# Performance work log

Hardware: AMD Instinct MI355X
Metric: run time of the kernel (lower is better)

The kernel has to match this reference:

```python
import jax, jax.numpy as jnp
import numpy as np


def setup_inputs() -> dict:
    key = jax.random.key(0)
    ks = jax.random.split(key, 10)
    B, C1, C2, Co, H, W = 4, 128, 128, 128, 64, 64
    Cin = C1 + C2
    delta_p_processed = jax.random.normal(ks[0], (B, C1, H, W), jnp.float32)
    delta_f_hist = jax.random.normal(ks[1], (B, C2, H, W), jnp.float32)
    Wq = jax.random.normal(ks[2], (Co, Cin), jnp.float32) * 0.02
    bq = jax.random.normal(ks[3], (Co,), jnp.float32) * 0.02
    Wk = jax.random.normal(ks[4], (Co, Cin), jnp.float32) * 0.02
    bk = jax.random.normal(ks[5], (Co,), jnp.float32) * 0.02
    Wv = jax.random.normal(ks[6], (Co, Cin), jnp.float32) * 0.02
    bv = jax.random.normal(ks[7], (Co,), jnp.float32) * 0.02
    Wg = jax.random.normal(ks[8], (Co, Co), jnp.float32) * 0.02
    bg = jnp.zeros((Co,), jnp.float32)
    gamma = jnp.array([0.5], jnp.float32)
    return {
        "delta_p_processed": delta_p_processed,
        "delta_f_hist": delta_f_hist,
        "Wq": Wq, "bq": bq, "Wk": Wk, "bk": bk,
        "Wv": Wv, "bv": bv, "Wg": Wg, "bg": bg,
        "gamma": gamma,
    }


def reference(delta_p_processed, delta_f_hist, Wq, bq, Wk, bk, Wv, bv, Wg, bg, gamma):
    x = jnp.concatenate([delta_p_processed, delta_f_hist], axis=1)  # (B, Cin, H, W)
    B, Cin, H, W = x.shape
    Co = Wq.shape[0]
    N = H * W
    xf = x.reshape(B, Cin, N)
    # 1x1 convs == per-pixel linear projections
    q = jnp.einsum('oc,bcn->bno', Wq, xf) + bq          # (B, N, Co)
    k = jnp.einsum('oc,bcn->bon', Wk, xf) + bk[:, None]  # (B, Co, N)
    v = jnp.einsum('oc,bcn->bno', Wv, xf) + bv          # (B, N, Co)
    scale = 1.0 / (Co ** 0.5)
    attn = jax.nn.softmax(jnp.einsum('bno,bom->bnm', q, k) * scale, axis=-1)  # (B, N, N)
    out_attn = jnp.einsum('bnm,bmo->bno', attn, v)      # (B, N, Co)
    out_attn = out_attn.transpose(0, 2, 1).reshape(B, Co, H, W)
    gate = jax.nn.sigmoid(
        jnp.einsum('oc,bchw->bohw', Wg, out_attn) + bg[None, :, None, None]
    )
    residual = x[:, :Co, :, :]
    return gamma[0] * gate * out_attn + (1.0 - gate) * residual
```

## Files before the change

### kernel.cpp

```cpp
#include <hip/hip_runtime.h>
#include <stdint.h>

#define B_    4
#define CIN   256
#define CO    128
#define NPOS  4096

typedef float  f4      __attribute__((ext_vector_type(4)));
typedef float  f2      __attribute__((ext_vector_type(2)));
typedef float  f32x16  __attribute__((ext_vector_type(16)));
typedef int    int4v   __attribute__((ext_vector_type(4)));
typedef short  short4v __attribute__((ext_vector_type(4)));
typedef short  short8v __attribute__((ext_vector_type(8)));
typedef __bf16 bf16x8  __attribute__((ext_vector_type(8)));

#if __has_builtin(__builtin_amdgcn_exp2f)
#define EXP2(x) __builtin_amdgcn_exp2f(x)
#else
#define EXP2(x) exp2f(x)
#endif

static __device__ __forceinline__ unsigned short f2bf(float f){
  union { float f; unsigned int u; } v; v.f = f;
  unsigned int u = v.u + 0x7FFFu + ((v.u >> 16) & 1u);
  return (unsigned short)(u >> 16);
}
static __device__ __forceinline__ float bf2f(unsigned short h){
  union { unsigned int u; float f; } v; v.u = ((unsigned int)h) << 16;
  return v.f;
}
static __device__ __forceinline__ unsigned int cvt_pk_bf16(float lo, float hi){
  unsigned int r;
  asm("v_cvt_pk_bf16_f32 %0, %1, %2" : "=v"(r) : "v"(lo), "v"(hi));
  return r;
}

static __device__ __forceinline__ void half_swap_pair(float v, float& x, float& y){
  union { float f; int i; } a; a.f = v;
  auto r = __builtin_amdgcn_permlane32_swap(a.i, a.i, false, false);
  union { int i; float f; } o0, o1; o0.i = (int)r[0]; o1.i = (int)r[1];
  x = o0.f; y = o1.f;
}

__global__ __launch_bounds__(64) void wconv_kernel(
    const float* __restrict__ Wq, const float* __restrict__ Wk,
    const float* __restrict__ Wv, const float* __restrict__ Wg,
    unsigned short* __restrict__ Wf)
{
  int blk = blockIdx.x, l = threadIdx.x;
  const float* W; int o, c; int stride;
  if (blk < 192){
    int ob = blk >> 4, cs = blk & 15;
    int mat = ob >> 2, obl = ob & 3;
    W = (mat == 0) ? Wq : ((mat == 1) ? Wk : Wv);
    o = obl * 32 + (l & 31); c = cs * 16 + (l >> 5) * 8; stride = 256;
  } else {
    int idx = blk - 192;
    int ob = idx >> 3, cs = idx & 7;
    W = Wg;
    o = ob * 32 + (l & 31); c = cs * 16 + (l >> 5) * 8; stride = 128;
  }
  const float* src = W + (size_t)o * stride + c;
  f4 a = *(const f4*)src, bb = *(const f4*)(src + 4);
  short8v pk;
  #pragma unroll
  for (int j = 0; j < 4; ++j){ pk[j] = (short)f2bf(a[j]); pk[4+j] = (short)f2bf(bb[j]); }
  *(short8v*)(Wf + ((size_t)blk * 64 + l) * 8) = pk;
}

__global__ __launch_bounds__(256) void qkv_kernel(
    const float* __restrict__ dp, const float* __restrict__ df,
    const unsigned short* __restrict__ Wf,
    const float* __restrict__ bq, const float* __restrict__ bk,
    const float* __restrict__ bv,
    unsigned short* __restrict__ Qf, unsigned short* __restrict__ Kf,
    unsigned short* __restrict__ Vf)
{
  __shared__ unsigned int xs4[32 * 128];

  int t  = threadIdx.x;
  int b  = blockIdx.x >> 7;
  int kt = blockIdx.x & 127;
  int n0 = kt * 32;

  {
    int cp = t & 127, nh = t >> 7;
    int c0 = cp * 2, c1 = c0 + 1;
    const float* s0 = (c0 < 128) ? dp + ((size_t)b*128 + c0) * NPOS
                                 : df + ((size_t)b*128 + (c0-128)) * NPOS;
    const float* s1 = (c1 < 128) ? dp + ((size_t)b*128 + c1) * NPOS
                                 : df + ((size_t)b*128 + (c1-128)) * NPOS;
    f4 x0[4], x1[4];
    #pragma unroll
    for (int i = 0; i < 4; ++i){
      x0[i] = *(const f4*)(s0 + n0 + nh*16 + i*4);
      x1[i] = *(const f4*)(s1 + n0 + nh*16 + i*4);
    }
    #pragma unroll
    for (int i = 0; i < 16; ++i){
      int n = nh * 16 + i;
      unsigned int pk = cvt_pk_bf16(x0[i>>2][i&3], x1[i>>2][i&3]);
      int chunk = (cp >> 2) ^ (n & 7);
      xs4[n * 128 + chunk * 4 + (cp & 3)] = pk;
    }
  }
  __syncthreads();

  int w = t >> 6, l = t & 63;
  int lo5 = l & 31, h = l >> 5;

  f32x16 acc[3] = {};
  const unsigned short* WfL = Wf + (size_t)l * 8;

  #pragma unroll 4
  for (int cs = 0; cs < 16; ++cs){
    bf16x8 xf = *(const bf16x8*)((const char*)xs4 +
                 (size_t)(lo5 * 512 + (((cs*2 + h) ^ (lo5 & 7)) * 16)));
    #pragma unroll
    for (int i = 0; i < 3; ++i){
      int ob = w * 3 + i;
      bf16x8 wf = *(const bf16x8*)(WfL + ((size_t)ob * 16 + cs) * 512);
      if (ob < 8) acc[i] = __builtin_amdgcn_mfma_f32_32x32x16_bf16(wf, xf, acc[i], 0, 0, 0);
      else        acc[i] = __builtin_amdgcn_mfma_f32_32x32x16_bf16(xf, wf, acc[i], 0, 0, 0);
    }
  }

  const float kScale = 0.12751743f;
  #pragma unroll
  for (int i = 0; i < 3; ++i){
    int ob = w * 3 + i, mat = ob >> 2, obl = ob & 3;
    if (mat < 2){
      const float* bias = (mat == 0) ? bq : bk;
      unsigned short* dst = ((mat == 0) ? Qf : Kf) + (size_t)(b*128 + kt) * 4096;
      #pragma unroll
      for (int r1 = 0; r1 < 4; ++r1){
        f4 b4 = *(const f4*)(bias + obl*32 + r1*8 + h*4);
        float v0 = acc[i][r1*4+0] + b4[0], v1 = acc[i][r1*4+1] + b4[1];
        float v2 = acc[i][r1*4+2] + b4[2], v3 = acc[i][r1*4+3] + b4[3];
        if (mat == 0){ v0 *= kScale; v1 *= kScale; v2 *= kScale; v3 *= kScale; }
        union { unsigned int u[2]; short4v s; } pk;
        pk.u[0] = cvt_pk_bf16(v0, v1); pk.u[1] = cvt_pk_bf16(v2, v3);
        int ci = obl * 2 + (r1 >> 1);
        size_t si = (size_t)ci * 512 + (size_t)(lo5 + 32*(r1 & 1)) * 8 + 4*h;
        *(short4v*)(dst + si) = pk.s;
      }
    } else {
      float bvl = bv[obl * 32 + lo5];
      unsigned short* dst = Vf + ((size_t)(b*128 + kt) * 8 + obl*2) * 512;
      #pragma unroll
      for (int r1 = 0; r1 < 4; ++r1){
        union { unsigned int u[2]; short4v s; } pk;
        pk.u[0] = cvt_pk_bf16(acc[i][r1*4+0] + bvl, acc[i][r1*4+1] + bvl);
        pk.u[1] = cvt_pk_bf16(acc[i][r1*4+2] + bvl, acc[i][r1*4+3] + bvl);
        size_t si = (size_t)(r1 >> 1) * 512 + (size_t)(lo5 + 32*(r1 & 1)) * 8 + 4*h;
        *(short4v*)(dst + si) = pk.s;
      }
    }
  }
}

#define ATTN_TILE(K0, CUR, NXT)                                                 \
  {                                                                             \
    f32x16 sA = {}, sB = {};                                                    \
    __builtin_amdgcn_s_setprio(1);                                              \
    _Pragma("unroll")                                                           \
    for (int ci = 0; ci < 4; ++ci){                                             \
      sA = __builtin_amdgcn_mfma_f32_32x32x16_bf16(kf[CUR][2*ci],   qf[2*ci],   sA, 0, 0, 0); \
      sB = __builtin_amdgcn_mfma_f32_32x32x16_bf16(kf[CUR][2*ci+1], qf[2*ci+1], sB, 0, 0, 0); \
    }                                                                           \
    __builtin_amdgcn_s_setprio(0);                                              \
                    \
    {                                                                           \
      int kn_ = (K0) + 32; if (kn_ >= kend) kn_ = kbeg;                         \
      size_t tb_ = (size_t)(kn_ >> 5) * 4096;                                   \
      _Pragma("unroll")                                                         \
      for (int ci = 0; ci < 8; ++ci)                                            \
        kf[NXT][ci] = *(const bf16x8*)(KfL + tb_ + ci * 512);                   \
      _Pragma("unroll")                                                         \
      for (int fi = 0; fi < 8; ++fi)                                            \
        vf[NXT][fi] = *(const bf16x8*)(VfL + tb_ + fi * 512);                   \
    }                                                                           \
    f32x16 sv = sA + sB;                                                        \
    float a0_ = fmaxf(fmaxf(sv[0],  sv[1]),  sv[2]);                            \
    float a1_ = fmaxf(fmaxf(sv[3],  sv[4]),  sv[5]);                            \
    float a2_ = fmaxf(fmaxf(sv[6],  sv[7]),  sv[8]);                            \
    float a3_ = fmaxf(fmaxf(sv[9],  sv[10]), sv[11]);                           \
    float a4_ = fmaxf(fmaxf(sv[12], sv[13]), sv[14]);                           \
    float vm  = fmaxf(fmaxf(fmaxf(fmaxf(a0_, a1_), a2_), fmaxf(a3_, a4_)), sv[15]); \
    { float xx_, yy_; half_swap_pair(vm, xx_, yy_);                             \
      vm = fmaxf(vm, fmaxf(xx_, yy_)); }                                        \
    if (!__all(vm <= m_run + 8.0f)){                                            \
      float m_new = fmaxf(m_run, vm);                                           \
      float alpha = EXP2(m_run - m_new);                                        \
      _Pragma("unroll")                                                         \
      for (int ob = 0; ob < 4; ++ob){                                           \
        _Pragma("unroll")                                                       \
        for (int i = 0; i < 16; ++i) oacc[ob][i] *= alpha;                      \
      }                                                                         \
      l_run *= alpha;                                                           \
      m_run = m_new;                                                            \
    }                                                                           \
    float p[16];                                                                \
    _Pragma("unroll")                                                           \
    for (int i = 0; i < 16; ++i) p[i] = EXP2(sv[i] - m_run);                    \
    float t0 = (p[0]  + p[1])  + (p[2]  + p[3]);                                \
    float t1 = (p[4]  + p[5])  + (p[6]  + p[7]);                                \
    float t2 = (p[8]  + p[9])  + (p[10] + p[11]);                               \
    float t3 = (p[12] + p[13]) + (p[14] + p[15]);                               \
    float ts = (t0 + t1) + (t2 + t3);                                           \
    { float xx_, yy_; half_swap_pair(ts, xx_, yy_); ts = xx_ + yy_; }           \
    l_run += ts;                                                                \
    unsigned int pw[8];                                                         \
    _Pragma("unroll")                                                           \
    for (int i = 0; i < 8; ++i) pw[i] = cvt_pk_bf16(p[2*i], p[2*i+1]);          \
    auto r20 = __builtin_amdgcn_permlane32_swap((int)pw[2], (int)pw[0], false, false); \
    auto r31 = __builtin_amdgcn_permlane32_swap((int)pw[3], (int)pw[1], false, false); \
    auto r64v = __builtin_amdgcn_permlane32_swap((int)pw[6], (int)pw[4], false, false); \
    auto r75 = __builtin_amdgcn_permlane32_swap((int)pw[7], (int)pw[5], false, false); \
    union { int4v i4; bf16x8 b; } pb0, pb1;                                     \
    pb0.i4 = (int4v){(int)r20[1],  (int)r31[1], (int)r20[0],  (int)r31[0]};     \
    pb1.i4 = (int4v){(int)r64v[1], (int)r75[1], (int)r64v[0], (int)r75[0]};     \
    __builtin_amdgcn_s_setprio(1);                                              \
    _Pragma("unroll")                                                           \
    for (int ob = 0; ob < 4; ++ob){                                             \
      oacc[ob] = __builtin_amdgcn_mfma_f32_32x32x16_bf16(vf[CUR][2*ob],   pb0.b, oacc[ob], 0, 0, 0); \
      oacc[ob] = __builtin_amdgcn_mfma_f32_32x32x16_bf16(vf[CUR][2*ob+1], pb1.b, oacc[ob], 0, 0, 0); \
    }                                                                           \
    __builtin_amdgcn_s_setprio(0);                                              \
  }

__global__ __launch_bounds__(256) void attn_kernel(
    const unsigned short* __restrict__ Qf, const unsigned short* __restrict__ Kf,
    const unsigned short* __restrict__ Vf, float* __restrict__ OP,
    f2* __restrict__ ML, int SPLIT, int CHUNK)
{
  int t    = threadIdx.x;
  int b    = blockIdx.x >> 7;
  int qb   = blockIdx.x & 127;
  int w    = t >> 6;
  int l    = t & 63;
  int lq   = l & 31;
  int h    = l >> 5;
  int q0   = qb * 32;
  int s    = w;

  const unsigned short* QfL = Qf + (size_t)b * (128 * 8 * 512) + (size_t)l * 8;
  size_t qtb = (size_t)qb * 4096;
  bf16x8 qf[8];
  #pragma unroll
  for (int ci = 0; ci < 8; ++ci) qf[ci] = *(const bf16x8*)(QfL + qtb + ci * 512);

  const unsigned short* KfL = Kf + (size_t)b * (128 * 8 * 512) + (size_t)l * 8;
  const unsigned short* VfL = Vf + (size_t)b * (128 * 8 * 512) + (size_t)l * 8;

  f32x16 oacc[4] = {};
  float m_run = -3.0e38f, l_run = 0.f;

  const int kbeg = s * CHUNK;
  const int kend = kbeg + CHUNK;

  bf16x8 kf[2][8];
  bf16x8 vf[2][8];
  {
    size_t tb0 = (size_t)(kbeg >> 5) * 4096;
    #pragma unroll
    for (int ci = 0; ci < 8; ++ci) kf[0][ci] = *(const bf16x8*)(KfL + tb0 + ci * 512);
    #pragma unroll
    for (int fi = 0; fi < 8; ++fi) vf[0][fi] = *(const bf16x8*)(VfL + tb0 + fi * 512);
  }

  const int NIT = CHUNK >> 5;
  for (int it = 0; it < NIT; it += 2){
    int k0a = kbeg + it * 32;
    ATTN_TILE(k0a, 0, 1)
    int k0b = k0a + 32;
    ATTN_TILE(k0b, 1, 0)
  }

  float* Ob = OP + (((size_t)b * NPOS + q0 + lq) * SPLIT + s) * 128 + h * 4;
  #pragma unroll
  for (int ob = 0; ob < 4; ++ob){
    #pragma unroll
    for (int rg = 0; rg < 4; ++rg){
      f4 vv;
      vv[0] = oacc[ob][rg*4+0]; vv[1] = oacc[ob][rg*4+1];
      vv[2] = oacc[ob][rg*4+2]; vv[3] = oacc[ob][rg*4+3];
      *(f4*)(Ob + ob * 32 + rg * 8) = vv;
    }
  }
  if (h == 0){
    f2 ml; ml[0] = m_run; ml[1] = l_run;
    ML[((size_t)b * NPOS + q0 + lq) * SPLIT + s] = ml;
  }
}

__global__ __launch_bounds__(256) void gate_kernel(
    const float* __restrict__ OP, const f2* __restrict__ ML,
    const unsigned short* __restrict__ Wf,
    const float* __restrict__ bg,
    const float* __restrict__ gamma, const float* __restrict__ dp,
    float* __restrict__ out, int SPLIT)
{
  __shared__ float        oat[128 * 33];
  __shared__ unsigned int xs[32 * 64];
  __shared__ float        wsm[32 * 8];

  int t  = threadIdx.x;
  int b  = blockIdx.x >> 7;
  int nt = blockIdx.x & 127;
  int n0 = nt * 32;

  if (t < 32){
    size_t mlb = ((size_t)b * NPOS + n0 + t) * SPLIT;
    float mmax = -3.0e38f;
    for (int sp = 0; sp < SPLIT; ++sp) mmax = fmaxf(mmax, ML[mlb + sp][0]);
    float L = 0.f;
    for (int sp = 0; sp < SPLIT; ++sp) L += ML[mlb + sp][1] * EXP2(ML[mlb + sp][0] - mmax);
    float Linv = 1.0f / L;
    for (int sp = 0; sp < SPLIT; ++sp)
      wsm[t * 8 + sp] = EXP2(ML[mlb + sp][0] - mmax) * Linv;
  }
  __syncthreads();

  int w = t >> 6, l = t & 63;

  #pragma unroll
  for (int i = 0; i < 8; ++i){
    int n = w * 8 + i;
    const f2* op = (const f2*)(OP + (((size_t)b * NPOS + n0 + n) * SPLIT) * 128) + l;
    float a0 = 0.f, a1 = 0.f;
    for (int sp = 0; sp < SPLIT; ++sp){
      f2 v = op[sp * 64];
      float ww = wsm[n * 8 + sp];
      a0 += ww * v[0]; a1 += ww * v[1];
    }
    oat[(2*l)   * 33 + n] = a0;
    oat[(2*l+1) * 33 + n] = a1;
    xs[n * 64 + (((l >> 2) ^ (n & 7)) << 2) + (l & 3)] = cvt_pk_bf16(a0, a1);
  }
  __syncthreads();

  int lq = l & 31, h = l >> 5;
  f32x16 acc = {};
  const unsigned short* WgfL = Wf + (size_t)(192 + w * 8) * 512 + (size_t)l * 8;
  #pragma unroll
  for (int cs = 0; cs < 8; ++cs){
    bf16x8 xf = *(const bf16x8*)((const char*)xs +
                 (size_t)(lq * 256 + (((cs*2 + h) ^ (lq & 7)) * 16)));
    bf16x8 wgf = *(const bf16x8*)(WgfL + (size_t)cs * 512);
    acc = __builtin_amdgcn_mfma_f32_32x32x16_bf16(wgf, xf, acc, 0, 0, 0);
  }

  float gm = gamma[0];
  const float kLog2e = 1.4426950408889634f;
  #pragma unroll
  for (int r1 = 0; r1 < 4; ++r1){
    f4 b4 = *(const f4*)(bg + w*32 + r1*8 + h*4);
    #pragma unroll
    for (int j = 0; j < 4; ++j){
      int o = w*32 + r1*8 + h*4 + j;
      float garg = acc[r1*4 + j] + b4[j];
      float gate = 1.0f / (1.0f + EXP2(-kLog2e * garg));
      float oa = oat[o * 33 + lq];
      size_t gi = ((size_t)b * 128 + o) * NPOS + n0 + lq;
      float rs = dp[gi];
      out[gi] = gm * gate * oa + (1.0f - gate) * rs;
    }
  }
}

extern "C" void kernel_launch(void* const* d_in, const int* in_sizes, int n_in,
                              void* d_out, int out_size, void* d_ws, size_t ws_size,
                              hipStream_t stream)
{
  (void)in_sizes; (void)n_in; (void)out_size;
  const float* dp    = (const float*)d_in[0];
  const float* df    = (const float*)d_in[1];
  const float* Wq    = (const float*)d_in[2];
  const float* bq    = (const float*)d_in[3];
  const float* Wk    = (const float*)d_in[4];
  const float* bk    = (const float*)d_in[5];
  const float* Wv    = (const float*)d_in[6];
  const float* bv    = (const float*)d_in[7];
  const float* Wg    = (const float*)d_in[8];
  const float* bg    = (const float*)d_in[9];
  const float* gamma = (const float*)d_in[10];

  const int SPLIT = 4;
  const int CHUNK = NPOS / SPLIT;

  unsigned short* Qf = (unsigned short*)d_ws;
  unsigned short* Kf = Qf + (size_t)B_ * NPOS * 128;
  unsigned short* Vf = Kf + (size_t)B_ * NPOS * 128;
  float*          OP = (float*)(Vf + (size_t)B_ * NPOS * 128);
  f2*             ML = (f2*)(OP + (size_t)B_ * NPOS * SPLIT * 128);
  unsigned short* Wf = (unsigned short*)(ML + (size_t)B_ * NPOS * SPLIT);
  float*          out = (float*)d_out;
  (void)ws_size;

  wconv_kernel<<<dim3(224), dim3(64), 0, stream>>>(Wq, Wk, Wv, Wg, Wf);
  qkv_kernel<<<dim3(B_ * 128), dim3(256), 0, stream>>>(dp, df, Wf, bq, bk, bv, Qf, Kf, Vf);
  attn_kernel<<<dim3(B_ * 128), dim3(256), 0, stream>>>(Qf, Kf, Vf, OP, ML, SPLIT, CHUNK);
  gate_kernel<<<dim3(B_ * 128), dim3(256), 0, stream>>>(OP, ML, Wf, bg, gamma, dp, out, SPLIT);
}
```

Before: 96.31 us.

## Process two query tiles per wave to reuse K/V fragments

The attention kernel now has each wave compute two 32-row query tiles against the same loaded K and V fragments, keeping separate softmax running stats and accumulators for each tile. This halves the K/V global loads per unit of MFMA work and interleaves independent MFMA chains. The grid is halved, so fewer waves run per CU, and register pressure roughly doubles, which could cause spills or lower occupancy.

```diff
diff --git a/kernel.cpp b/kernel.cpp
--- a/kernel.cpp
+++ b/kernel.cpp
@@ -159,14 +159,16 @@
   }
 }
 
-#define ATTN_TILE(K0, CUR, NXT)                                                 \
+#define ATTN_TILE2(K0, CUR, NXT)                                                \
   {                                                                             \
-    f32x16 sA = {}, sB = {};                                                    \
+    f32x16 sA0 = {}, sB0 = {}, sA1 = {}, sB1 = {};                              \
     __builtin_amdgcn_s_setprio(1);                                              \
     _Pragma("unroll")                                                           \
     for (int ci = 0; ci < 4; ++ci){                                             \
-      sA = __builtin_amdgcn_mfma_f32_32x32x16_bf16(kf[CUR][2*ci],   qf[2*ci],   sA, 0, 0, 0); \
-      sB = __builtin_amdgcn_mfma_f32_32x32x16_bf16(kf[CUR][2*ci+1], qf[2*ci+1], sB, 0, 0, 0); \
+      sA0 = __builtin_amdgcn_mfma_f32_32x32x16_bf16(kf[CUR][2*ci],   qf0[2*ci],   sA0, 0, 0, 0); \
+      sA1 = __builtin_amdgcn_mfma_f32_32x32x16_bf16(kf[CUR][2*ci],   qf1[2*ci],   sA1, 0, 0, 0); \
+      sB0 = __builtin_amdgcn_mfma_f32_32x32x16_bf16(kf[CUR][2*ci+1], qf0[2*ci+1], sB0, 0, 0, 0); \
+      sB1 = __builtin_amdgcn_mfma_f32_32x32x16_bf16(kf[CUR][2*ci+1], qf1[2*ci+1], sB1, 0, 0, 0); \
     }                                                                           \
     __builtin_amdgcn_s_setprio(0);                                              \
                     \
@@ -180,51 +182,92 @@
       for (int fi = 0; fi < 8; ++fi)                                            \
         vf[NXT][fi] = *(const bf16x8*)(VfL + tb_ + fi * 512);                   \
     }                                                                           \
-    f32x16 sv = sA + sB;                                                        \
-    float a0_ = fmaxf(fmaxf(sv[0],  sv[1]),  sv[2]);                            \
-    float a1_ = fmaxf(fmaxf(sv[3],  sv[4]),  sv[5]);                            \
-    float a2_ = fmaxf(fmaxf(sv[6],  sv[7]),  sv[8]);                            \
-    float a3_ = fmaxf(fmaxf(sv[9],  sv[10]), sv[11]);                           \
-    float a4_ = fmaxf(fmaxf(sv[12], sv[13]), sv[14]);                           \
-    float vm  = fmaxf(fmaxf(fmaxf(fmaxf(a0_, a1_), a2_), fmaxf(a3_, a4_)), sv[15]); \
-    { float xx_, yy_; half_swap_pair(vm, xx_, yy_);                             \
-      vm = fmaxf(vm, fmaxf(xx_, yy_)); }                                        \
-    if (!__all(vm <= m_run + 8.0f)){                                            \
-      float m_new = fmaxf(m_run, vm);                                           \
-      float alpha = EXP2(m_run - m_new);                                        \
+    f32x16 sv0 = sA0 + sB0, sv1 = sA1 + sB1;                                    \
+                                      \
+    float vm0, vm1;                                                             \
+    { float a0_ = fmaxf(fmaxf(sv0[0],  sv0[1]),  sv0[2]);                       \
+      float a1_ = fmaxf(fmaxf(sv0[3],  sv0[4]),  sv0[5]);                       \
+      float a2_ = fmaxf(fmaxf(sv0[6],  sv0[7]),  sv0[8]);                       \
+      float a3_ = fmaxf(fmaxf(sv0[9],  sv0[10]), sv0[11]);                      \
+      float a4_ = fmaxf(fmaxf(sv0[12], sv0[13]), sv0[14]);                      \
+      vm0 = fmaxf(fmaxf(fmaxf(fmaxf(a0_, a1_), a2_), fmaxf(a3_, a4_)), sv0[15]); } \
+    { float a0_ = fmaxf(fmaxf(sv1[0],  sv1[1]),  sv1[2]);                       \
+      float a1_ = fmaxf(fmaxf(sv1[3],  sv1[4]),  sv1[5]);                       \
+      float a2_ = fmaxf(fmaxf(sv1[6],  sv1[7]),  sv1[8]);                       \
+      float a3_ = fmaxf(fmaxf(sv1[9],  sv1[10]), sv1[11]);                      \
+      float a4_ = fmaxf(fmaxf(sv1[12], sv1[13]), sv1[14]);                      \
+      vm1 = fmaxf(fmaxf(fmaxf(fmaxf(a0_, a1_), a2_), fmaxf(a3_, a4_)), sv1[15]); } \
+    { float xx_, yy_; half_swap_pair(vm0, xx_, yy_); vm0 = fmaxf(vm0, fmaxf(xx_, yy_)); } \
+    { float xx_, yy_; half_swap_pair(vm1, xx_, yy_); vm1 = fmaxf(vm1, fmaxf(xx_, yy_)); } \
+    if (!__all(vm0 <= m0 + 8.0f)){                                              \
+      float m_new = fmaxf(m0, vm0);                                             \
+      float alpha = EXP2(m0 - m_new);                                           \
       _Pragma("unroll")                                                         \
       for (int ob = 0; ob < 4; ++ob){                                           \
         _Pragma("unroll")                                                       \
-        for (int i = 0; i < 16; ++i) oacc[ob][i] *= alpha;                      \
+        for (int i = 0; i < 16; ++i) acc0[ob][i] *= alpha;                      \
       }                                                                         \
-      l_run *= alpha;                                                           \
-      m_run = m_new;                                                            \
-    }                                                                           \
-    float p[16];                                                                \
+      l0 *= alpha; m0 = m_new;                                                  \
+    }                                                                           \
+    if (!__all(vm1 <= m1 + 8.0f)){                                              \
+      float m_new = fmaxf(m1, vm1);                                             \
+      float alpha = EXP2(m1 - m_new);                                           \
+      _Pragma("unroll")                                                         \
+      for (int ob = 0; ob < 4; ++ob){                                           \
+        _Pragma("unroll")                                                       \
+        for (int i = 0; i < 16; ++i) acc1[ob][i] *= alpha;                      \
+      }                                                                         \
+      l1 *= alpha; m1 = m_new;                                                  \
+    }                                                                           \
+    float p0[16], p1[16];                                                       \
     _Pragma("unroll")                                                           \
-    for (int i = 0; i < 16; ++i) p[i] = EXP2(sv[i] - m_run);                    \
-    float t0 = (p[0]  + p[1])  + (p[2]  + p[3]);                                \
-    float t1 = (p[4]  + p[5])  + (p[6]  + p[7]);                                \
-    float t2 = (p[8]  + p[9])  + (p[10] + p[11]);                               \
-    float t3 = (p[12] + p[13]) + (p[14] + p[15]);                               \
-    float ts = (t0 + t1) + (t2 + t3);                                           \
-    { float xx_, yy_; half_swap_pair(ts, xx_, yy_); ts = xx_ + yy_; }           \
-    l_run += ts;                                                                \
-    unsigned int pw[8];                                                         \
-    _Pragma("unroll")                                                           \
-    for (int i = 0; i < 8; ++i) pw[i] = cvt_pk_bf16(p[2*i], p[2*i+1]);          \
-    auto r20 = __builtin_amdgcn_permlane32_swap((int)pw[2], (int)pw[0], false, false); \
-    auto r31 = __builtin_amdgcn_permlane32_swap((int)pw[3], (int)pw[1], false, false); \
-    auto r64v = __builtin_amdgcn_permlane32_swap((int)pw[6], (int)pw[4], false, false); \
-    auto r75 = __builtin_amdgcn_permlane32_swap((int)pw[7], (int)pw[5], false, false); \
-    union { int4v i4; bf16x8 b; } pb0, pb1;                                     \
-    pb0.i4 = (int4v){(int)r20[1],  (int)r31[1], (int)r20[0],  (int)r31[0]};     \
-    pb1.i4 = (int4v){(int)r64v[1], (int)r75[1], (int)r64v[0], (int)r75[0]};     \
+    for (int i = 0; i < 16; ++i){ p0[i] = EXP2(sv0[i] - m0); p1[i] = EXP2(sv1[i] - m1); } \
+    { float t0 = (p0[0]+p0[1])+(p0[2]+p0[3]);                                   \
+      float t1 = (p0[4]+p0[5])+(p0[6]+p0[7]);                                   \
+      float t2 = (p0[8]+p0[9])+(p0[10]+p0[11]);                                 \
+      float t3 = (p0[12]+p0[13])+(p0[14]+p0[15]);                               \
+      float ts = (t0+t1)+(t2+t3);                                               \
+      float xx_, yy_; half_swap_pair(ts, xx_, yy_); l0 += xx_ + yy_; }          \
+    { float t0 = (p1[0]+p1[1])+(p1[2]+p1[3]);                                   \
+      float t1 = (p1[4]+p1[5])+(p1[6]+p1[7]);                                   \
+      float t2 = (p1[8]+p1[9])+(p1[10]+p1[11]);                                 \
+      float t3 = (p1[12]+p1[13])+(p1[14]+p1[15]);                               \
+      float ts = (t0+t1)+(t2+t3);                                               \
+      float xx_, yy_; half_swap_pair(ts, xx_, yy_); l1 += xx_ + yy_; }          \
+    bf16x8 q0pb0, q0pb1, q1pb0, q1pb1;                                          \
+    {                                                                           \
+      unsigned int pw[8];                                                       \
+      _Pragma("unroll")                                                         \
+      for (int i = 0; i < 8; ++i) pw[i] = cvt_pk_bf16(p0[2*i], p0[2*i+1]);      \
+      auto r20 = __builtin_amdgcn_permlane32_swap((int)pw[2], (int)pw[0], false, false); \
+      auto r31 = __builtin_amdgcn_permlane32_swap((int)pw[3], (int)pw[1], false, false); \
+      auto r64v = __builtin_amdgcn_permlane32_swap((int)pw[6], (int)pw[4], false, false); \
+      auto r75 = __builtin_amdgcn_permlane32_swap((int)pw[7], (int)pw[5], false, false); \
+      union { int4v i4; bf16x8 b; } u0, u1;                                     \
+      u0.i4 = (int4v){(int)r20[1],  (int)r31[1], (int)r20[0],  (int)r31[0]};    \
+      u1.i4 = (int4v){(int)r64v[1], (int)r75[1], (int)r64v[0], (int)r75[0]};    \
+      q0pb0 = u0.b; q0pb1 = u1.b;                                               \
+    }                                                                           \
+    {                                                                           \
+      unsigned int pw[8];                                                       \
+      _Pragma("unroll")                                                         \
+      for (int i = 0; i < 8; ++i) pw[i] = cvt_pk_bf16(p1[2*i], p1[2*i+1]);      \
+      auto r20 = __builtin_amdgcn_permlane32_swap((int)pw[2], (int)pw[0], false, false); \
+      auto r31 = __builtin_amdgcn_permlane32_swap((int)pw[3], (int)pw[1], false, false); \
+      auto r64v = __builtin_amdgcn_permlane32_swap((int)pw[6], (int)pw[4], false, false); \
+      auto r75 = __builtin_amdgcn_permlane32_swap((int)pw[7], (int)pw[5], false, false); \
+      union { int4v i4; bf16x8 b; } u0, u1;                                     \
+      u0.i4 = (int4v){(int)r20[1],  (int)r31[1], (int)r20[0],  (int)r31[0]};    \
+      u1.i4 = (int4v){(int)r64v[1], (int)r75[1], (int)r64v[0], (int)r75[0]};    \
+      q1pb0 = u0.b; q1pb1 = u1.b;                                               \
+    }                                                                           \
     __builtin_amdgcn_s_setprio(1);                                              \
     _Pragma("unroll")                                                           \
     for (int ob = 0; ob < 4; ++ob){                                             \
-      oacc[ob] = __builtin_amdgcn_mfma_f32_32x32x16_bf16(vf[CUR][2*ob],   pb0.b, oacc[ob], 0, 0, 0); \
-      oacc[ob] = __builtin_amdgcn_mfma_f32_32x32x16_bf16(vf[CUR][2*ob+1], pb1.b, oacc[ob], 0, 0, 0); \
+      acc0[ob] = __builtin_amdgcn_mfma_f32_32x32x16_bf16(vf[CUR][2*ob],   q0pb0, acc0[ob], 0, 0, 0); \
+      acc1[ob] = __builtin_amdgcn_mfma_f32_32x32x16_bf16(vf[CUR][2*ob],   q1pb0, acc1[ob], 0, 0, 0); \
+      acc0[ob] = __builtin_amdgcn_mfma_f32_32x32x16_bf16(vf[CUR][2*ob+1], q0pb1, acc0[ob], 0, 0, 0); \
+      acc1[ob] = __builtin_amdgcn_mfma_f32_32x32x16_bf16(vf[CUR][2*ob+1], q1pb1, acc1[ob], 0, 0, 0); \
     }                                                                           \
     __builtin_amdgcn_s_setprio(0);                                              \
   }
@@ -235,26 +278,33 @@
     f2* __restrict__ ML, int SPLIT, int CHUNK)
 {
   int t    = threadIdx.x;
-  int b    = blockIdx.x >> 7;
-  int qb   = blockIdx.x & 127;
+  int b    = blockIdx.x >> 6;
+  int qt   = blockIdx.x & 63;
   int w    = t >> 6;
   int l    = t & 63;
   int lq   = l & 31;
   int h    = l >> 5;
-  int q0   = qb * 32;
+  int q0   = qt * 64;
   int s    = w;
 
   const unsigned short* QfL = Qf + (size_t)b * (128 * 8 * 512) + (size_t)l * 8;
-  size_t qtb = (size_t)qb * 4096;
-  bf16x8 qf[8];
-  #pragma unroll
-  for (int ci = 0; ci < 8; ++ci) qf[ci] = *(const bf16x8*)(QfL + qtb + ci * 512);
+  bf16x8 qf0[8], qf1[8];
+  {
+    size_t qtb0 = (size_t)(qt * 2)     * 4096;
+    size_t qtb1 = (size_t)(qt * 2 + 1) * 4096;
+    #pragma unroll
+    for (int ci = 0; ci < 8; ++ci){
+      qf0[ci] = *(const bf16x8*)(QfL + qtb0 + ci * 512);
+      qf1[ci] = *(const bf16x8*)(QfL + qtb1 + ci * 512);
+    }
+  }
 
   const unsigned short* KfL = Kf + (size_t)b * (128 * 8 * 512) + (size_t)l * 8;
   const unsigned short* VfL = Vf + (size_t)b * (128 * 8 * 512) + (size_t)l * 8;
 
-  f32x16 oacc[4] = {};
-  float m_run = -3.0e38f, l_run = 0.f;
+  f32x16 acc0[4] = {}, acc1[4] = {};
+  float m0 = -3.0e38f, l0 = 0.f;
+  float m1 = -3.0e38f, l1 = 0.f;
 
   const int kbeg = s * CHUNK;
   const int kend = kbeg + CHUNK;
@@ -272,25 +322,35 @@
   const int NIT = CHUNK >> 5;
   for (int it = 0; it < NIT; it += 2){
     int k0a = kbeg + it * 32;
-    ATTN_TILE(k0a, 0, 1)
+    ATTN_TILE2(k0a, 0, 1)
     int k0b = k0a + 32;
-    ATTN_TILE(k0b, 1, 0)
-  }
-
-  float* Ob = OP + (((size_t)b * NPOS + q0 + lq) * SPLIT + s) * 128 + h * 4;
-  #pragma unroll
-  for (int ob = 0; ob < 4; ++ob){
-    #pragma unroll
-    for (int rg = 0; rg < 4; ++rg){
-      f4 vv;
-      vv[0] = oacc[ob][rg*4+0]; vv[1] = oacc[ob][rg*4+1];
-      vv[2] = oacc[ob][rg*4+2]; vv[3] = oacc[ob][rg*4+3];
-      *(f4*)(Ob + ob * 32 + rg * 8) = vv;
+    ATTN_TILE2(k0b, 1, 0)
+  }
+
+  #pragma unroll
+  for (int qs = 0; qs < 2; ++qs){
+    float* Ob = OP + (((size_t)b * NPOS + q0 + qs * 32 + lq) * SPLIT + s) * 128 + h * 4;
+    #pragma unroll
+    for (int ob = 0; ob < 4; ++ob){
+      #pragma unroll
+      for (int rg = 0; rg < 4; ++rg){
+        f4 vv;
+        if (qs == 0){
+          vv[0] = acc0[ob][rg*4+0]; vv[1] = acc0[ob][rg*4+1];
+          vv[2] = acc0[ob][rg*4+2]; vv[3] = acc0[ob][rg*4+3];
+        } else {
+          vv[0] = acc1[ob][rg*4+0]; vv[1] = acc1[ob][rg*4+1];
+          vv[2] = acc1[ob][rg*4+2]; vv[3] = acc1[ob][rg*4+3];
+        }
+        *(f4*)(Ob + ob * 32 + rg * 8) = vv;
+      }
     }
   }
   if (h == 0){
-    f2 ml; ml[0] = m_run; ml[1] = l_run;
-    ML[((size_t)b * NPOS + q0 + lq) * SPLIT + s] = ml;
+    f2 ml0; ml0[0] = m0; ml0[1] = l0;
+    ML[((size_t)b * NPOS + q0 + lq) * SPLIT + s] = ml0;
+    f2 ml1; ml1[0] = m1; ml1[1] = l1;
+    ML[((size_t)b * NPOS + q0 + 32 + lq) * SPLIT + s] = ml1;
   }
 }
 
@@ -400,6 +460,6 @@
 
   wconv_kernel<<<dim3(224), dim3(64), 0, stream>>>(Wq, Wk, Wv, Wg, Wf);
   qkv_kernel<<<dim3(B_ * 128), dim3(256), 0, stream>>>(dp, df, Wf, bq, bk, bv, Qf, Kf, Vf);
-  attn_kernel<<<dim3(B_ * 128), dim3(256), 0, stream>>>(Qf, Kf, Vf, OP, ML, SPLIT, CHUNK);
+  attn_kernel<<<dim3(B_ * 64), dim3(256), 0, stream>>>(Qf, Kf, Vf, OP, ML, SPLIT, CHUNK);
   gate_kernel<<<dim3(B_ * 128), dim3(256), 0, stream>>>(OP, ML, Wf, bg, gamma, dp, out, SPLIT);
 }
```

Measured after the change: 155.1 us. 1.61x slower.
